# Kernel optimization log

Hardware: AMD Instinct MI355X
Metric: run time of the kernel (lower is better)

Reference implementation:

```python
import jax, jax.numpy as jnp
import numpy as np

K0 = 16                       # probe slice length (hard-coded in kernel)
TAU = 2.053748910631823       # t-test threshold (|tau| of kernel constant)


def setup_inputs() -> dict:
    key = jax.random.key(0)
    k1, k2, k3 = jax.random.split(key, 3)
    B, DIN, DOUT = 8192, 4096, 4096
    x = jax.random.normal(k1, (B, DIN), dtype=jnp.float32)
    W = jax.random.normal(k2, (DOUT, DIN), dtype=jnp.float32)
    bias = jax.random.normal(k3, (DOUT,), dtype=jnp.float32)
    return {"x": x, "W": W, "bias": bias}


def reference(x, W, bias):
    # --- partial dot over the first K0 columns of K (the probe) ---
    x0 = x[:, :K0]                    # [B, K0]
    w0 = W[:, :K0]                    # [DOUT, K0]
    y1 = x0 @ w0.T                    # [B, DOUT]  sum_k x_k * w_k
    # sum of squared elementwise products: prod_k^2 = x_k^2 * w_k^2
    s2 = (x0 * x0) @ (w0 * w0).T      # [B, DOUT]
    # --- per-(row, column) t-statistic and early-exit decision ---
    tstat = jnp.abs(y1) / jnp.sqrt(s2 / K0)
    passed = tstat < TAU              # True -> column deemed insignificant, zeroed
    # --- full linear (active columns keep full accumulation + bias) ---
    full = x @ W.T + bias[None, :]    # [B, DOUT]
    return jnp.where(passed, 0.0, full)
```

## Files before the change

kernel.cpp:

```cpp
#include <hip/hip_runtime.h>
#include <cstdint>
#include <cstddef>

#define TAU_D 2.053748910631823
#define M_DIM 8192
#define N_DIM 4096
#define K_DIM 4096
#define NIT   32

typedef float f32x4  __attribute__((ext_vector_type(4)));
typedef short bf16x8 __attribute__((ext_vector_type(8)));

typedef __attribute__((address_space(1))) void gvoid_t;
typedef __attribute__((address_space(3))) void lvoid_t;

__device__ __forceinline__ void gload_lds16(const void* g, void* l) {
    __builtin_amdgcn_global_load_lds((const gvoid_t*)g, (lvoid_t*)l, 16, 0, 0);
}

__device__ __forceinline__ unsigned int pack2bf(float lo, float hi) {
    unsigned int ul = __float_as_uint(lo);
    unsigned int uh = __float_as_uint(hi);
    ul = (ul + 0x7FFFu + ((ul >> 16) & 1u)) >> 16;
    uh = (uh + 0x7FFFu + ((uh >> 16) & 1u)) >> 16;
    return ul | (uh << 16);
}

__global__ void cvt_f32_to_bf16(const float4* __restrict__ in,
                                uint2* __restrict__ out, int n4) {
    int i = blockIdx.x * blockDim.x + threadIdx.x;
    const int stride = gridDim.x * blockDim.x;
    for (; i < n4; i += stride) {
        float4 a = in[i];
        uint2 o;
        o.x = pack2bf(a.x, a.y);
        o.y = pack2bf(a.z, a.w);
        out[i] = o;
    }
}

#define BAR() do { __builtin_amdgcn_s_barrier(); \
                   asm volatile("" ::: "memory"); } while (0)

__global__ __launch_bounds__(512, 2) void gemm_masked8(
    const unsigned short* __restrict__ Ab,
    const unsigned short* __restrict__ Bb,
    const float* __restrict__ X,
    const float* __restrict__ Wt,
    const float* __restrict__ bias,
    float* __restrict__ out)
{
    __shared__ __align__(16) char lds[131072];

    const int tid  = threadIdx.x;
    const int wave = tid >> 6;
    const int lane = tid & 63;
    const int lr = lane & 15;
    const int lq = lane >> 4;
    const int wm = wave >> 2;
    const int wn = wave & 3;

    const int flat = blockIdx.x;
    const int xcd  = flat & 7;
    const int s    = flat >> 3;
    const int rnd  = s >> 5;
    const int jj   = s & 31;
    const int trow = rnd * 16 + ((xcd >> 2) << 3) + (jj >> 2);
    const int tcol = ((xcd & 3) << 2) + (jj & 3);
    const int rowBase = trow * 256;
    const int colBase = tcol * 256;

    f32x4 acc[8][4];
    #pragma unroll
    for (int i = 0; i < 8; ++i)
        #pragma unroll
        for (int n = 0; n < 4; ++n)
            acc[i][n] = (f32x4){0.f, 0.f, 0.f, 0.f};

    const int srow  = tid >> 3;
    const int sslot = (tid & 7) ^ (srow & 7);
    const unsigned short* aSrc =
        Ab + (size_t)(rowBase + srow) * K_DIM + sslot * 8;
    const unsigned short* bSrc =
        Bb + (size_t)(colBase + srow) * K_DIM + sslot * 8;

    const unsigned R0A = 0, R0B = 32768, R1A = 65536, R1B = 98304;

    auto stageHalfA = [&](int kst, unsigned reg, int h) {
        #pragma unroll
        for (int i = 2 * h; i < 2 * h + 2; ++i)
            gload_lds16(aSrc + (size_t)i * 64 * K_DIM + kst * 64,
                        lds + reg + i * 8192 + wave * 1024);
    };
    auto stageHalfB = [&](int kst, unsigned reg, int h) {
        #pragma unroll
        for (int i = 2 * h; i < 2 * h + 2; ++i)
            gload_lds16(bSrc + (size_t)i * 64 * K_DIM + kst * 64,
                        lds + reg + i * 8192 + wave * 1024);
    };

    const unsigned kk0 = (unsigned)((lq) ^ (lr & 7)) * 16;
    const unsigned kk1 = (unsigned)((4 + lq) ^ (lr & 7)) * 16;
    const unsigned rowA = (unsigned)(wm * 128 + lr) * 128;
    const unsigned rowB = (unsigned)(wn * 64 + lr) * 128;

    stageHalfA(0, R0A, 0); stageHalfA(0, R0A, 1);
    stageHalfB(0, R0B, 0); stageHalfB(0, R0B, 1);
    stageHalfB(1, R1B, 0); stageHalfB(1, R1B, 1);
    asm volatile("s_waitcnt vmcnt(4)" ::: "memory");
    BAR();

    bf16x8 aF[4][2];
    bf16x8 bF0[2][2];
    bf16x8 bF1[2][2];

    #define MFMA_QUAD(ACC_M, ACC_N, BREG)                                      \
        do {                                                                   \
            __builtin_amdgcn_s_setprio(1);                                     \
            _Pragma("unroll")                                                  \
            for (int m = 0; m < 4; ++m)                                        \
                _Pragma("unroll")                                              \
                for (int n = 0; n < 2; ++n)                                    \
                    _Pragma("unroll")                                          \
                    for (int ks = 0; ks < 2; ++ks)                             \
                        acc[(ACC_M) + m][(ACC_N) + n] =                        \
                            __builtin_amdgcn_mfma_f32_16x16x32_bf16(           \
                                aF[m][ks], BREG[n][ks],                        \
                                acc[(ACC_M) + m][(ACC_N) + n], 0, 0, 0);       \
            __builtin_amdgcn_s_setprio(0);                                     \
        } while (0)

    for (int j = 0; j < NIT; ++j) {
        const int ka = 2 * j;
        const int kb = 2 * j + 1;
        const bool stg = (j + 1 < NIT);

        #pragma unroll
        for (int m = 0; m < 4; ++m) {
            aF[m][0] = *(const bf16x8*)(lds + R0A + rowA + m * 2048 + kk0);
            aF[m][1] = *(const bf16x8*)(lds + R0A + rowA + m * 2048 + kk1);
        }
        #pragma unroll
        for (int n = 0; n < 2; ++n) {
            bF0[n][0] = *(const bf16x8*)(lds + R0B + rowB + n * 2048 + kk0);
            bF0[n][1] = *(const bf16x8*)(lds + R0B + rowB + n * 2048 + kk1);
        }
        stageHalfA(kb, R1A, 0);
        BAR();
        MFMA_QUAD(0, 0, bF0);

        #pragma unroll
        for (int n = 0; n < 2; ++n) {
            bF1[n][0] = *(const bf16x8*)(lds + R0B + rowB + (2 + n) * 2048 + kk0);
            bF1[n][1] = *(const bf16x8*)(lds + R0B + rowB + (2 + n) * 2048 + kk1);
        }
        stageHalfA(kb, R1A, 1);
        BAR();
        MFMA_QUAD(0, 2, bF1);

        #pragma unroll
        for (int m = 0; m < 4; ++m) {
            aF[m][0] = *(const bf16x8*)(lds + R0A + rowA + (4 + m) * 2048 + kk0);
            aF[m][1] = *(const bf16x8*)(lds + R0A + rowA + (4 + m) * 2048 + kk1);
        }
        BAR();
        MFMA_QUAD(4, 2, bF1);

        if (stg) {
            stageHalfB(ka + 2, R0B, 0);
            asm volatile("s_waitcnt vmcnt(2)" ::: "memory");
        } else {
            asm volatile("s_waitcnt vmcnt(0)" ::: "memory");
        }
        BAR();
        MFMA_QUAD(4, 0, bF0);

        #pragma unroll
        for (int m = 0; m < 4; ++m) {
            aF[m][0] = *(const bf16x8*)(lds + R1A + rowA + m * 2048 + kk0);
            aF[m][1] = *(const bf16x8*)(lds + R1A + rowA + m * 2048 + kk1);
        }
        #pragma unroll
        for (int n = 0; n < 2; ++n) {
            bF0[n][0] = *(const bf16x8*)(lds + R1B + rowB + n * 2048 + kk0);
            bF0[n][1] = *(const bf16x8*)(lds + R1B + rowB + n * 2048 + kk1);
        }
        if (stg) stageHalfB(ka + 2, R0B, 1);
        BAR();
        MFMA_QUAD(0, 0, bF0);

        #pragma unroll
        for (int n = 0; n < 2; ++n) {
            bF1[n][0] = *(const bf16x8*)(lds + R1B + rowB + (2 + n) * 2048 + kk0);
            bF1[n][1] = *(const bf16x8*)(lds + R1B + rowB + (2 + n) * 2048 + kk1);
        }
        if (stg) stageHalfA(ka + 2, R0A, 0);
        BAR();
        MFMA_QUAD(0, 2, bF1);

        #pragma unroll
        for (int m = 0; m < 4; ++m) {
            aF[m][0] = *(const bf16x8*)(lds + R1A + rowA + (4 + m) * 2048 + kk0);
            aF[m][1] = *(const bf16x8*)(lds + R1A + rowA + (4 + m) * 2048 + kk1);
        }
        if (stg) stageHalfA(ka + 2, R0A, 1);
        BAR();
        MFMA_QUAD(4, 2, bF1);

        if (stg) {
            stageHalfB(kb + 2, R1B, 0);
            stageHalfB(kb + 2, R1B, 1);
            asm volatile("s_waitcnt vmcnt(4)" ::: "memory");
        }
        BAR();
        MFMA_QUAD(4, 0, bF0);
    }

    __syncthreads();
    float* x0s = (float*)(lds);
    float* w0s = (float*)(lds + 16384);
    #pragma unroll
    for (int i = 0; i < 2; ++i) {
        int idx = tid + i * 512;
        int r = idx >> 2, qq = (idx & 3) << 2;
        *(f32x4*)(x0s + r * 16 + qq) =
            *(const f32x4*)(X + (size_t)(rowBase + r) * K_DIM + qq);
        *(f32x4*)(w0s + r * 16 + qq) =
            *(const f32x4*)(Wt + (size_t)(colBase + r) * K_DIM + qq);
    }
    __syncthreads();

    const float TAU32 = (float)TAU_D;

    #pragma unroll
    for (int np = 0; np < 4; np += 2) {
        float wv[2][16];
        float bv[2];
        #pragma unroll
        for (int e = 0; e < 2; ++e) {
            const int c = wn * 64 + (np + e) * 16 + lr;
            #pragma unroll
            for (int q = 0; q < 4; ++q)
                *(f32x4*)&wv[e][q * 4] = *(const f32x4*)(w0s + c * 16 + q * 4);
            bv[e] = bias[colBase + c];
        }
        #pragma unroll
        for (int mi = 0; mi < 8; ++mi) {
            #pragma unroll
            for (int jr = 0; jr < 4; ++jr) {
                const int rw = wm * 128 + mi * 16 + lq * 4 + jr;
                float xv[16];
                #pragma unroll
                for (int q = 0; q < 4; ++q)
                    *(f32x4*)&xv[q * 4] = *(const f32x4*)(x0s + rw * 16 + q * 4);
                const size_t orow = (size_t)(rowBase + rw) * N_DIM + colBase;
                #pragma unroll
                for (int e = 0; e < 2; ++e) {
                    const int n = np + e;
                    float y1 = 0.f, s2 = 0.f;
                    #pragma unroll
                    for (int k = 0; k < 16; ++k) {
                        float xk = xv[k], wk = wv[e][k];
                        float xx = xk * xk, ww = wk * wk;
                        y1 = fmaf(xk, wk, y1);
                        s2 = fmaf(xx, ww, s2);
                    }
                    float t = fabsf(y1) / sqrtf(s2 * 0.0625f);
                    float v = (t < TAU32) ? 0.0f : (acc[mi][n][jr] + bv[e]);
                    out[orow + wn * 64 + n * 16 + lr] = v;
                }
            }
        }
    }
}

__global__ __launch_bounds__(256, 2) void gemm_masked_fb(
    const float* __restrict__ X, const float* __restrict__ Wt,
    const float* __restrict__ bias, float* __restrict__ out)
{
    __shared__ __align__(16) unsigned short As[128 * 32];
    __shared__ __align__(16) unsigned short Bs[128 * 32];

    const int tid  = threadIdx.x;
    const int wave = tid >> 6;
    const int lane = tid & 63;
    const int rowBase = blockIdx.y * 128;
    const int colBase = blockIdx.x * 128;
    const int wr = wave >> 1;
    const int wc = wave & 1;
    const int lr = lane & 15;
    const int lq = lane >> 4;

    f32x4 acc[4][4];
    #pragma unroll
    for (int m = 0; m < 4; ++m)
        #pragma unroll
        for (int n = 0; n < 4; ++n)
            acc[m][n] = (f32x4){0.f, 0.f, 0.f, 0.f};

    const int srow = tid >> 2;
    const int scol = (tid & 3) * 8;
    const float* afp = X  + (size_t)(rowBase + srow) * K_DIM + scol;
    const float* bfp = Wt + (size_t)(colBase + srow) * K_DIM + scol;

    for (int kt = 0; kt < K_DIM; kt += 32) {
        #pragma unroll
        for (int issue = 0; issue < 2; ++issue) {
            const float* sa = afp + (size_t)issue * 64 * K_DIM;
            const float* sb = bfp + (size_t)issue * 64 * K_DIM;
            float4 a0 = *(const float4*)(sa);
            float4 a1 = *(const float4*)(sa + 4);
            float4 b0 = *(const float4*)(sb);
            float4 b1 = *(const float4*)(sb + 4);
            uint4 pa, pb;
            pa.x = pack2bf(a0.x, a0.y); pa.y = pack2bf(a0.z, a0.w);
            pa.z = pack2bf(a1.x, a1.y); pa.w = pack2bf(a1.z, a1.w);
            pb.x = pack2bf(b0.x, b0.y); pb.y = pack2bf(b0.z, b0.w);
            pb.z = pack2bf(b1.x, b1.y); pb.w = pack2bf(b1.z, b1.w);
            *(uint4*)((char*)As + issue * 4096 + tid * 16) = pa;
            *(uint4*)((char*)Bs + issue * 4096 + tid * 16) = pb;
        }
        afp += 32; bfp += 32;
        __syncthreads();

        bf16x8 af[4], bq[4];
        #pragma unroll
        for (int m = 0; m < 4; ++m)
            af[m] = *(const bf16x8*)(As + (wr * 64 + m * 16 + lr) * 32 + lq * 8);
        #pragma unroll
        for (int n = 0; n < 4; ++n)
            bq[n] = *(const bf16x8*)(Bs + (wc * 64 + n * 16 + lr) * 32 + lq * 8);
        #pragma unroll
        for (int m = 0; m < 4; ++m)
            #pragma unroll
            for (int n = 0; n < 4; ++n)
                acc[m][n] = __builtin_amdgcn_mfma_f32_16x16x32_bf16(
                    af[m], bq[n], acc[m][n], 0, 0, 0);
        __syncthreads();
    }

    float* x0s = (float*)As;
    float* w0s = (float*)Bs;
    #pragma unroll
    for (int i = 0; i < 2; ++i) {
        int idx = tid + i * 256;
        int r = idx >> 2, q = (idx & 3) * 4;
        *(float4*)(x0s + r * 16 + q) =
            *(const float4*)(X + (size_t)(rowBase + r) * K_DIM + q);
        *(float4*)(w0s + r * 16 + q) =
            *(const float4*)(Wt + (size_t)(colBase + r) * K_DIM + q);
    }
    __syncthreads();

    const float TAU32 = (float)TAU_D;
    float wv[4][16];
    float bv[4];
    #pragma unroll
    for (int n = 0; n < 4; ++n) {
        int c = wc * 64 + n * 16 + lr;
        #pragma unroll
        for (int q = 0; q < 4; ++q)
            *(f32x4*)&wv[n][q * 4] = *(const f32x4*)(w0s + c * 16 + q * 4);
        bv[n] = bias[colBase + c];
    }

    #pragma unroll
    for (int m = 0; m < 4; ++m) {
        #pragma unroll
        for (int j = 0; j < 4; ++j) {
            const int r = wr * 64 + m * 16 + lq * 4 + j;
            float xv[16];
            #pragma unroll
            for (int q = 0; q < 4; ++q)
                *(f32x4*)&xv[q * 4] = *(const f32x4*)(x0s + r * 16 + q * 4);
            const size_t orow = (size_t)(rowBase + r) * N_DIM + colBase;
            #pragma unroll
            for (int n = 0; n < 4; ++n) {
                float y1 = 0.f, s2 = 0.f;
                #pragma unroll
                for (int k = 0; k < 16; ++k) {
                    float xk = xv[k];
                    float wk = wv[n][k];
                    float xx = xk * xk;
                    float ww = wk * wk;
                    y1 = fmaf(xk, wk, y1);
                    s2 = fmaf(xx, ww, s2);
                }
                float t = fabsf(y1) / sqrtf(s2 * 0.0625f);
                float v = (t < TAU32) ? 0.0f : (acc[m][n][j] + bv[n]);
                out[orow + wc * 64 + n * 16 + lr] = v;
            }
        }
    }
}

extern "C" void kernel_launch(void* const* d_in, const int* in_sizes, int n_in,
                              void* d_out, int out_size, void* d_ws, size_t ws_size,
                              hipStream_t stream) {
    const float* x    = (const float*)d_in[0];
    const float* W    = (const float*)d_in[1];
    const float* bias = (const float*)d_in[2];
    float* out = (float*)d_out;

    const size_t needA = (size_t)M_DIM * K_DIM * 2;
    const size_t needB = (size_t)N_DIM * K_DIM * 2;

    if (ws_size >= needA + needB) {
        unsigned short* xb = (unsigned short*)d_ws;
        unsigned short* wb = (unsigned short*)((char*)d_ws + needA);
        cvt_f32_to_bf16<<<2048, 256, 0, stream>>>(
            (const float4*)x, (uint2*)xb, (M_DIM * K_DIM) / 4);
        cvt_f32_to_bf16<<<2048, 256, 0, stream>>>(
            (const float4*)W, (uint2*)wb, (N_DIM * K_DIM) / 4);
        dim3 grid((M_DIM / 256) * (N_DIM / 256));
        gemm_masked8<<<grid, 512, 0, stream>>>(xb, wb, x, W, bias, out);
    } else {
        dim3 grid(N_DIM / 128, M_DIM / 128);
        gemm_masked_fb<<<grid, 256, 0, stream>>>(x, W, bias, out);
    }
}
```

Measured before the change: 307.4 us.

## Restructure GEMM main loop into four phases with full B-fragment loads

The K-loop's eight fine-grained phases, each running MFMA quadrants on 2 B fragments, become four phases that load all 4 B fragments and run a half-tile of MFMAs (4x4x2). Staging of A and B tiles is issued in whole-tile chunks rather than halves, which halves the barrier count per iteration. This cuts barrier and scheduling overhead. In exchange it holds more B-fragment registers live and gives coarser interleaving of global-to-LDS loads with compute, which could expose memory latency or raise register pressure.

```diff
diff --git a/kernel.cpp b/kernel.cpp
--- a/kernel.cpp
+++ b/kernel.cpp
@@ -86,15 +86,15 @@
 
     const unsigned R0A = 0, R0B = 32768, R1A = 65536, R1B = 98304;
 
-    auto stageHalfA = [&](int kst, unsigned reg, int h) {
-        #pragma unroll
-        for (int i = 2 * h; i < 2 * h + 2; ++i)
+    auto stageA = [&](int kst, unsigned reg) {
+        #pragma unroll
+        for (int i = 0; i < 4; ++i)
             gload_lds16(aSrc + (size_t)i * 64 * K_DIM + kst * 64,
                         lds + reg + i * 8192 + wave * 1024);
     };
-    auto stageHalfB = [&](int kst, unsigned reg, int h) {
-        #pragma unroll
-        for (int i = 2 * h; i < 2 * h + 2; ++i)
+    auto stageB = [&](int kst, unsigned reg) {
+        #pragma unroll
+        for (int i = 0; i < 4; ++i)
             gload_lds16(bSrc + (size_t)i * 64 * K_DIM + kst * 64,
                         lds + reg + i * 8192 + wave * 1024);
     };
@@ -104,29 +104,28 @@
     const unsigned rowA = (unsigned)(wm * 128 + lr) * 128;
     const unsigned rowB = (unsigned)(wn * 64 + lr) * 128;
 
-    stageHalfA(0, R0A, 0); stageHalfA(0, R0A, 1);
-    stageHalfB(0, R0B, 0); stageHalfB(0, R0B, 1);
-    stageHalfB(1, R1B, 0); stageHalfB(1, R1B, 1);
+    stageA(0, R0A);
+    stageB(0, R0B);
+    stageB(1, R1B);
     asm volatile("s_waitcnt vmcnt(4)" ::: "memory");
     BAR();
 
     bf16x8 aF[4][2];
-    bf16x8 bF0[2][2];
-    bf16x8 bF1[2][2];
-
-    #define MFMA_QUAD(ACC_M, ACC_N, BREG)                                      \
+    bf16x8 bF[4][2];
+
+    #define MFMA_HALF(ACC_M)                                                   \
         do {                                                                   \
             __builtin_amdgcn_s_setprio(1);                                     \
             _Pragma("unroll")                                                  \
             for (int m = 0; m < 4; ++m)                                        \
                 _Pragma("unroll")                                              \
-                for (int n = 0; n < 2; ++n)                                    \
+                for (int n = 0; n < 4; ++n)                                    \
                     _Pragma("unroll")                                          \
                     for (int ks = 0; ks < 2; ++ks)                             \
-                        acc[(ACC_M) + m][(ACC_N) + n] =                        \
+                        acc[(ACC_M) + m][n] =                                  \
                             __builtin_amdgcn_mfma_f32_16x16x32_bf16(           \
-                                aF[m][ks], BREG[n][ks],                        \
-                                acc[(ACC_M) + m][(ACC_N) + n], 0, 0, 0);       \
+                                aF[m][ks], bF[n][ks],                          \
+                                acc[(ACC_M) + m][n], 0, 0, 0);                 \
             __builtin_amdgcn_s_setprio(0);                                     \
         } while (0)
 
@@ -141,39 +140,27 @@
             aF[m][1] = *(const bf16x8*)(lds + R0A + rowA + m * 2048 + kk1);
         }
         #pragma unroll
-        for (int n = 0; n < 2; ++n) {
-            bF0[n][0] = *(const bf16x8*)(lds + R0B + rowB + n * 2048 + kk0);
-            bF0[n][1] = *(const bf16x8*)(lds + R0B + rowB + n * 2048 + kk1);
-        }
-        stageHalfA(kb, R1A, 0);
+        for (int n = 0; n < 4; ++n) {
+            bF[n][0] = *(const bf16x8*)(lds + R0B + rowB + n * 2048 + kk0);
+            bF[n][1] = *(const bf16x8*)(lds + R0B + rowB + n * 2048 + kk1);
+        }
+        stageA(kb, R1A);
         BAR();
-        MFMA_QUAD(0, 0, bF0);
-
-        #pragma unroll
-        for (int n = 0; n < 2; ++n) {
-            bF1[n][0] = *(const bf16x8*)(lds + R0B + rowB + (2 + n) * 2048 + kk0);
-            bF1[n][1] = *(const bf16x8*)(lds + R0B + rowB + (2 + n) * 2048 + kk1);
-        }
-        stageHalfA(kb, R1A, 1);
-        BAR();
-        MFMA_QUAD(0, 2, bF1);
+        MFMA_HALF(0);
 
         #pragma unroll
         for (int m = 0; m < 4; ++m) {
             aF[m][0] = *(const bf16x8*)(lds + R0A + rowA + (4 + m) * 2048 + kk0);
             aF[m][1] = *(const bf16x8*)(lds + R0A + rowA + (4 + m) * 2048 + kk1);
         }
-        BAR();
-        MFMA_QUAD(4, 2, bF1);
-
         if (stg) {
-            stageHalfB(ka + 2, R0B, 0);
-            asm volatile("s_waitcnt vmcnt(2)" ::: "memory");
+            stageB(ka + 2, R0B);
+            asm volatile("s_waitcnt vmcnt(4)" ::: "memory");
         } else {
             asm volatile("s_waitcnt vmcnt(0)" ::: "memory");
         }
         BAR();
-        MFMA_QUAD(4, 0, bF0);
+        MFMA_HALF(4);
 
         #pragma unroll
         for (int m = 0; m < 4; ++m) {
@@ -181,39 +168,25 @@
             aF[m][1] = *(const bf16x8*)(lds + R1A + rowA + m * 2048 + kk1);
         }
         #pragma unroll
-        for (int n = 0; n < 2; ++n) {
-            bF0[n][0] = *(const bf16x8*)(lds + R1B + rowB + n * 2048 + kk0);
-            bF0[n][1] = *(const bf16x8*)(lds + R1B + rowB + n * 2048 + kk1);
-        }
-        if (stg) stageHalfB(ka + 2, R0B, 1);
+        for (int n = 0; n < 4; ++n) {
+            bF[n][0] = *(const bf16x8*)(lds + R1B + rowB + n * 2048 + kk0);
+            bF[n][1] = *(const bf16x8*)(lds + R1B + rowB + n * 2048 + kk1);
+        }
+        if (stg) stageA(ka + 2, R0A);
         BAR();
-        MFMA_QUAD(0, 0, bF0);
-
-        #pragma unroll
-        for (int n = 0; n < 2; ++n) {
-            bF1[n][0] = *(const bf16x8*)(lds + R1B + rowB + (2 + n) * 2048 + kk0);
-            bF1[n][1] = *(const bf16x8*)(lds + R1B + rowB + (2 + n) * 2048 + kk1);
-        }
-        if (stg) stageHalfA(ka + 2, R0A, 0);
-        BAR();
-        MFMA_QUAD(0, 2, bF1);
+        MFMA_HALF(0);
 
         #pragma unroll
         for (int m = 0; m < 4; ++m) {
             aF[m][0] = *(const bf16x8*)(lds + R1A + rowA + (4 + m) * 2048 + kk0);
             aF[m][1] = *(const bf16x8*)(lds + R1A + rowA + (4 + m) * 2048 + kk1);
         }
-        if (stg) stageHalfA(ka + 2, R0A, 1);
+        if (stg) {
+            stageB(kb + 2, R1B);
+            asm volatile("s_waitcnt vmcnt(4)" ::: "memory");
+        }
         BAR();
-        MFMA_QUAD(4, 2, bF1);
-
-        if (stg) {
-            stageHalfB(kb + 2, R1B, 0);
-            stageHalfB(kb + 2, R1B, 1);
-            asm volatile("s_waitcnt vmcnt(4)" ::: "memory");
-        }
-        BAR();
-        MFMA_QUAD(4, 0, bF0);
+        MFMA_HALF(4);
     }
 
     __syncthreads();
```

After: 311.9 us. About the same (+1.4%).
